# Kernel tuning notes

Hardware: AMD Instinct MI355X
Metric: run time of the kernel (lower is better)

Reference implementation:

```python
import jax, jax.numpy as jnp
import numpy as np

D, H, W, VP = 10, 400, 352, 35  # grid depth/height/width, points per voxel
C1_IN, C1_H = 7, 16   # VFE-1: Linear 7->16, concat -> 32
C2_IN, C2_H = 32, 64  # VFE-2: Linear 32->64, concat -> 128
BN_EPS = 1e-5


def setup_inputs() -> dict:
    key = jax.random.key(0)
    ks = jax.random.split(key, 12)
    K = 15000
    feature = jax.random.normal(ks[0], (K, VP, C1_IN), jnp.float32)
    keep = (jax.random.uniform(ks[1], (K, VP, 1)) < 0.8).astype(jnp.float32)
    feature = feature * keep
    bs = 1
    coordinate = jnp.concatenate([
        jax.random.randint(ks[2], (K, 1), 0, bs),
        jax.random.randint(ks[3], (K, 1), 0, D),
        jax.random.randint(ks[4], (K, 1), 0, H),
        jax.random.randint(ks[5], (K, 1), 0, W),
    ], axis=1).astype(jnp.int32)
    w1 = jax.random.normal(ks[6], (C1_IN, C1_H), jnp.float32) * 0.3
    b1 = jnp.zeros((C1_H,), jnp.float32)
    g1 = jnp.ones((C1_H,), jnp.float32)
    be1 = jnp.zeros((C1_H,), jnp.float32)
    w2 = jax.random.normal(ks[7], (C2_IN, C2_H), jnp.float32) * 0.15
    b2 = jnp.zeros((C2_H,), jnp.float32)
    g2 = jnp.ones((C2_H,), jnp.float32)
    be2 = jnp.zeros((C2_H,), jnp.float32)
    return dict(feature=feature, coordinate=coordinate, bs=bs,
                w1=w1, b1=b1, g1=g1, be1=be1,
                w2=w2, b2=b2, g2=g2, be2=be2)


def _vfe(x, mask, Wm, b, gamma, beta):
    # Linear + ReLU, then BatchNorm1d (training-mode batch stats over (K, VP))
    pw = jax.nn.relu(jnp.einsum('kpi,ih->kph', x, Wm) + b)
    mean = jnp.mean(pw, axis=(0, 1))
    var = jnp.var(pw, axis=(0, 1))  # biased variance, as BN uses for normalization
    pw = (pw - mean) * jax.lax.rsqrt(var + BN_EPS) * gamma + beta
    agg = jnp.max(pw, axis=1, keepdims=True)            # [K,1,Ch] per-voxel max
    concat = jnp.concatenate([pw, jnp.broadcast_to(agg, pw.shape)], axis=-1)
    return concat * mask                                  # mask broadcasts [K,VP,1]


def reference(feature, coordinate, bs, w1, b1, g1, be1, w2, b2, g2, be2):
    # mask: point is valid if max over its 7 features != 0
    mask = (jnp.max(feature, axis=2, keepdims=True) != 0).astype(feature.dtype)
    x = _vfe(feature, mask, w1, b1, g1, be1)   # [K,VP,32]
    x = _vfe(x, mask, w2, b2, g2, be2)         # [K,VP,128]
    voxelwise = jnp.max(x, axis=1)             # [K,128]
    c = coordinate
    out = jnp.zeros((bs, D, H, W, 2 * C2_H), feature.dtype)
    # sparse -> dense sums duplicate coordinates, matching torch.sparse to_dense
    out = out.at[c[:, 0], c[:, 1], c[:, 2], c[:, 3]].add(voxelwise)
    return out
```

## Files before the change

kernel.cpp:

```cpp
#include <hip/hip_runtime.h>
#include <math.h>

#define VPTS 35
#define CIN1 7
#define CH1  16
#define CH2  64
#define DD   10
#define HHH  400
#define WWW  352
#define BN_EPS 1e-5f
#define NSTRIPE 8


__global__ void __launch_bounds__(256) k_stats1(
    const float* __restrict__ feat,
    const float* __restrict__ w1, const float* __restrict__ b1,
    float* __restrict__ red1p, int KP) {
  float w[CIN1][CH1], bb[CH1];
#pragma unroll
  for (int i = 0; i < CIN1; ++i)
#pragma unroll
    for (int c = 0; c < CH1; ++c) w[i][c] = w1[i * CH1 + c];
#pragma unroll
  for (int c = 0; c < CH1; ++c) bb[c] = b1[c];
  float s[CH1], q[CH1];
#pragma unroll
  for (int c = 0; c < CH1; ++c) { s[c] = 0.f; q[c] = 0.f; }
  int tid = blockIdx.x * blockDim.x + threadIdx.x;
  int stride = gridDim.x * blockDim.x;
  for (int idx = tid; idx < KP; idx += stride) {
    float x[CIN1];
#pragma unroll
    for (int i = 0; i < CIN1; ++i) x[i] = feat[(size_t)idx * CIN1 + i];
#pragma unroll
    for (int c = 0; c < CH1; ++c) {
      float a = bb[c];
#pragma unroll
      for (int i = 0; i < CIN1; ++i) a = fmaf(x[i], w[i][c], a);
      a = fmaxf(a, 0.f);
      s[c] += a;
      q[c] = fmaf(a, a, q[c]);
    }
  }
  __shared__ float ssum[2 * CH1];
  if (threadIdx.x < 2 * CH1) ssum[threadIdx.x] = 0.f;
  __syncthreads();
#pragma unroll
  for (int c = 0; c < CH1; ++c) {
    float a = s[c], b = q[c];
    for (int o = 32; o > 0; o >>= 1) {
      a += __shfl_down(a, o);
      b += __shfl_down(b, o);
    }
    if ((threadIdx.x & 63) == 0) {
      atomicAdd(&ssum[c], a);
      atomicAdd(&ssum[CH1 + c], b);
    }
  }
  __syncthreads();
  if (threadIdx.x < 2 * CH1)
    atomicAdd(&red1p[(blockIdx.x & (NSTRIPE - 1)) * 2 * CH1 + threadIdx.x],
              ssum[threadIdx.x]);
}

__global__ void __launch_bounds__(256) k_heavy(
    const float* __restrict__ feat,
    const float* __restrict__ w1, const float* __restrict__ b1,
    const float* __restrict__ g1, const float* __restrict__ be1,
    const float* __restrict__ red1p,
    const float* __restrict__ w2, const float* __restrict__ b2,
    const float* __restrict__ g2,
    float* __restrict__ red2p,
    float* __restrict__ E1buf, float* __restrict__ E2buf,
    float* __restrict__ FLbuf, int K, float invN) {
  __shared__ __align__(16) float fs_s[4][248];
  __shared__ __align__(16) float pw1_s[4][560];
  __shared__ __align__(16) float agg1_s[4][16];
  __shared__ float ss[2 * CH2];
  int t = threadIdx.x, lane = t & 63, w = t >> 6;
  float* fs   = fs_s[w];
  float* pw1  = pw1_s[w];
  float* agg1 = agg1_s[w];

  int c1 = lane & 15;
  float r1s = 0.f, r1q = 0.f;
#pragma unroll
  for (int sIdx = 0; sIdx < NSTRIPE; ++sIdx) {
    r1s += red1p[sIdx * 2 * CH1 + c1];
    r1q += red1p[sIdx * 2 * CH1 + CH1 + c1];
  }
  float mean1 = r1s * invN;
  float var1  = r1q * invN - mean1 * mean1;
  float sc1   = g1[c1] * rsqrtf(var1 + BN_EPS);
  float sh1   = be1[c1] - mean1 * sc1;
  float b1c   = b1[c1];
  float w1r[CIN1];
#pragma unroll
  for (int j = 0; j < CIN1; ++j) w1r[j] = w1[j * CH1 + c1];
  float wcol[32];
#pragma unroll
  for (int i = 0; i < 32; ++i) wcol[i] = w2[i * CH2 + lane];
  float b2c = b2[lane];
  float sgn = (g2[lane] >= 0.f) ? 1.f : -1.f;

  float lsum = 0.f, lsq = 0.f;
  int waveg = blockIdx.x * 4 + w;
  int nwave = gridDim.x * 4;
  for (int k = waveg; k < K; k += nwave) {
    for (int i = lane; i < VPTS * CIN1; i += 64)
      fs[i] = feat[(size_t)k * (VPTS * CIN1) + i];
    bool vbit = false;
    if (lane < VPTS) {
      float m = fs[lane * CIN1];
#pragma unroll
      for (int j = 1; j < CIN1; ++j) m = fmaxf(m, fs[lane * CIN1 + j]);
      vbit = (m != 0.f);
    }
    unsigned long long mbits = __ballot(vbit);
#pragma unroll
    for (int j = 0; j < 9; ++j) {
      int idx = lane + 64 * j;
      if (idx < VPTS * CH1) {
        int p = idx >> 4;
        float a = b1c;
#pragma unroll
        for (int jj = 0; jj < CIN1; ++jj) a = fmaf(fs[p * CIN1 + jj], w1r[jj], a);
        a = fmaxf(a, 0.f);
        pw1[idx] = fmaf(a, sc1, sh1);
      }
    }
    {
      int g = lane >> 4;
      float am = -INFINITY;
      for (int p = g; p < VPTS; p += 4) am = fmaxf(am, pw1[p * CH1 + c1]);
      am = fmaxf(am, __shfl_xor(am, 16));
      am = fmaxf(am, __shfl_xor(am, 32));
      if (lane < CH1) agg1[lane] = am;
    }
    float aggdot = 0.f;
    {
      const float4* a4 = (const float4*)agg1;
#pragma unroll
      for (int i = 0; i < 4; ++i) {
        float4 v = a4[i];
        aggdot = fmaf(v.x, wcol[16 + 4 * i + 0], aggdot);
        aggdot = fmaf(v.y, wcol[16 + 4 * i + 1], aggdot);
        aggdot = fmaf(v.z, wcol[16 + 4 * i + 2], aggdot);
        aggdot = fmaf(v.w, wcol[16 + 4 * i + 3], aggdot);
      }
    }
    float E1w = -INFINITY, E2w = -INFINITY;
    const float4* p4 = (const float4*)pw1;
    for (int p = 0; p < VPTS; ++p) {
      float4 v0 = p4[p * 4 + 0], v1 = p4[p * 4 + 1];
      float4 v2 = p4[p * 4 + 2], v3 = p4[p * 4 + 3];
      float low = 0.f;
      low = fmaf(v0.x, wcol[0], low);  low = fmaf(v0.y, wcol[1], low);
      low = fmaf(v0.z, wcol[2], low);  low = fmaf(v0.w, wcol[3], low);
      low = fmaf(v1.x, wcol[4], low);  low = fmaf(v1.y, wcol[5], low);
      low = fmaf(v1.z, wcol[6], low);  low = fmaf(v1.w, wcol[7], low);
      low = fmaf(v2.x, wcol[8], low);  low = fmaf(v2.y, wcol[9], low);
      low = fmaf(v2.z, wcol[10], low); low = fmaf(v2.w, wcol[11], low);
      low = fmaf(v3.x, wcol[12], low); low = fmaf(v3.y, wcol[13], low);
      low = fmaf(v3.z, wcol[14], low); low = fmaf(v3.w, wcol[15], low);
      bool valid = (mbits >> p) & 1ull;
      float m = valid ? 1.f : 0.f;
      float pw2 = fmaxf(fmaf(m, low + aggdot, b2c), 0.f);
      lsum += pw2;
      lsq = fmaf(pw2, pw2, lsq);
      float sp = sgn * pw2;
      E2w = fmaxf(E2w, sp);
      if (valid) E1w = fmaxf(E1w, sp);
    }
    E1buf[(size_t)k * 64 + lane] = E1w;
    E2buf[(size_t)k * 64 + lane] = E2w;
    if (lane == 0) FLbuf[k] = (float)__popcll(mbits);
  }
  if (t < 2 * CH2) ss[t] = 0.f;
  __syncthreads();
  atomicAdd(&ss[lane], lsum);
  atomicAdd(&ss[CH2 + lane], lsq);
  __syncthreads();
  if (t < 2 * CH2)
    atomicAdd(&red2p[(blockIdx.x & (NSTRIPE - 1)) * 2 * CH2 + t], ss[t]);
}

__global__ void __launch_bounds__(256) k_scatter(
    const float* __restrict__ E1buf, const float* __restrict__ E2buf,
    const float* __restrict__ FLbuf, const float* __restrict__ red2p,
    const float* __restrict__ g2, const float* __restrict__ be2,
    const int* __restrict__ coord, float* __restrict__ out, int K,
    float invN) {
  __shared__ float scsh2_s[2 * CH2];
  int t = threadIdx.x;
  if (t < CH2) {
    float rs = 0.f, rq = 0.f;
#pragma unroll
    for (int sIdx = 0; sIdx < NSTRIPE; ++sIdx) {
      rs += red2p[sIdx * 2 * CH2 + t];
      rq += red2p[sIdx * 2 * CH2 + CH2 + t];
    }
    float mean = rs * invN;
    float var = rq * invN - mean * mean;
    float inv = rsqrtf(var + BN_EPS);
    float sc = g2[t] * inv;
    scsh2_s[t] = sc;
    scsh2_s[CH2 + t] = be2[t] - mean * sc;
  }
  __syncthreads();
  int k = blockIdx.x * 2 + (t >> 7);
  if (k >= K) return;
  int tl = t & 127;
  int c = tl & 63;
  float nv = FLbuf[k];
  bool anyV = nv > 0.f;
  bool anyI = nv < (float)VPTS;
  float sc = scsh2_s[c], sh = scsh2_s[CH2 + c];
  float cand = -INFINITY;
  if (anyV) {
    float E = (tl < 64) ? E1buf[(size_t)k * 64 + c] : E2buf[(size_t)k * 64 + c];
    cand = fmaf(fabsf(sc), E, sh);
  }
  if (anyI) cand = fmaxf(cand, 0.f);
  int4 cc = *reinterpret_cast<const int4*>(coord + (size_t)k * 4);
  long vox = ((long)(cc.x * DD + cc.y) * HHH + cc.z) * WWW + cc.w;
  atomicAdd(&out[vox * (2 * CH2) + tl], cand);
}

__global__ void k_finalize(const float* __restrict__ red,
                           const float* __restrict__ g,
                           const float* __restrict__ be,
                           float* __restrict__ scsh, int CH, float invN) {
  int c = threadIdx.x;
  if (c < CH) {
    float mean = red[c] * invN;
    float var = red[CH + c] * invN - mean * mean;
    float inv = rsqrtf(var + BN_EPS);
    float sc = g[c] * inv;
    scsh[c] = sc;
    scsh[CH + c] = be[c] - mean * sc;
  }
}

__global__ void __launch_bounds__(256) k_stats1_fb(
    const float* __restrict__ feat,
    const float* __restrict__ w1, const float* __restrict__ b1,
    float* __restrict__ red1, int KP) {
  float w[CIN1][CH1], bb[CH1];
#pragma unroll
  for (int i = 0; i < CIN1; ++i)
#pragma unroll
    for (int c = 0; c < CH1; ++c) w[i][c] = w1[i * CH1 + c];
#pragma unroll
  for (int c = 0; c < CH1; ++c) bb[c] = b1[c];
  float s[CH1], q[CH1];
#pragma unroll
  for (int c = 0; c < CH1; ++c) { s[c] = 0.f; q[c] = 0.f; }
  int tid = blockIdx.x * blockDim.x + threadIdx.x;
  int stride = gridDim.x * blockDim.x;
  for (int idx = tid; idx < KP; idx += stride) {
    float x[CIN1];
#pragma unroll
    for (int i = 0; i < CIN1; ++i) x[i] = feat[(size_t)idx * CIN1 + i];
#pragma unroll
    for (int c = 0; c < CH1; ++c) {
      float a = bb[c];
#pragma unroll
      for (int i = 0; i < CIN1; ++i) a = fmaf(x[i], w[i][c], a);
      a = fmaxf(a, 0.f);
      s[c] += a;
      q[c] = fmaf(a, a, q[c]);
    }
  }
  __shared__ float ssum[2 * CH1];
  if (threadIdx.x < 2 * CH1) ssum[threadIdx.x] = 0.f;
  __syncthreads();
#pragma unroll
  for (int c = 0; c < CH1; ++c) {
    float a = s[c], b = q[c];
    for (int o = 32; o > 0; o >>= 1) {
      a += __shfl_down(a, o);
      b += __shfl_down(b, o);
    }
    if ((threadIdx.x & 63) == 0) {
      atomicAdd(&ssum[c], a);
      atomicAdd(&ssum[CH1 + c], b);
    }
  }
  __syncthreads();
  if (threadIdx.x < 2 * CH1) atomicAdd(&red1[threadIdx.x], ssum[threadIdx.x]);
}

__device__ __forceinline__ void compute_x2_old(
    const float* __restrict__ feat, int k, int t,
    const float* __restrict__ w1, const float* __restrict__ b1,
    const float* __restrict__ scsh1,
    float* fs, float* mask_s, float* pw1_s, float* agg1_s, float* x2_s) {
  if (t < VPTS * CIN1) fs[t] = feat[(size_t)k * (VPTS * CIN1) + t];
  __syncthreads();
  if (t < VPTS) {
    float m = fs[t * CIN1];
#pragma unroll
    for (int i = 1; i < CIN1; ++i) m = fmaxf(m, fs[t * CIN1 + i]);
    mask_s[t] = (m != 0.f) ? 1.f : 0.f;
  }
  for (int i = t; i < VPTS * CH1; i += 256) {
    int p = i >> 4, c = i & 15;
    float acc = b1[c];
#pragma unroll
    for (int j = 0; j < CIN1; ++j) acc = fmaf(fs[p * CIN1 + j], w1[j * CH1 + c], acc);
    acc = fmaxf(acc, 0.f);
    pw1_s[i] = fmaf(acc, scsh1[c], scsh1[CH1 + c]);
  }
  __syncthreads();
  if (t < CH1) {
    float m = pw1_s[t];
    for (int p = 1; p < VPTS; ++p) m = fmaxf(m, pw1_s[p * CH1 + t]);
    agg1_s[t] = m;
  }
  __syncthreads();
  for (int i = t; i < VPTS * 32; i += 256) {
    int p = i >> 5, c = i & 31;
    x2_s[i] = (c < CH1 ? pw1_s[p * CH1 + c] : agg1_s[c - CH1]) * mask_s[p];
  }
  __syncthreads();
}

__global__ void __launch_bounds__(256) k_stats2_old(
    const float* __restrict__ feat,
    const float* __restrict__ w1, const float* __restrict__ b1,
    const float* __restrict__ scsh1,
    const float* __restrict__ w2, const float* __restrict__ b2,
    float* __restrict__ red2, int K) {
  __shared__ float fs[VPTS * CIN1], mask_s[VPTS], pw1_s[VPTS * CH1], agg1_s[CH1];
  __shared__ __align__(16) float x2_s[VPTS * 32];
  __shared__ __align__(16) float w2_s[32 * CH2];
  __shared__ float ss[2 * CH2];
  int t = threadIdx.x;
  for (int i = t; i < 32 * CH2; i += 256) w2_s[i] = w2[i];
  if (t < 2 * CH2) ss[t] = 0.f;
  __syncthreads();
  int c = t & 63;
  float wcol[32];
#pragma unroll
  for (int i = 0; i < 32; ++i) wcol[i] = w2_s[i * CH2 + c];
  float bb = b2[c];
  float lsum = 0.f, lsq = 0.f;
  for (int k = blockIdx.x; k < K; k += gridDim.x) {
    compute_x2_old(feat, k, t, w1, b1, scsh1, fs, mask_s, pw1_s, agg1_s, x2_s);
    for (int p = t >> 6; p < VPTS; p += 4) {
      const float4* xv = (const float4*)(x2_s + p * 32);
      float a = bb;
#pragma unroll
      for (int i = 0; i < 8; ++i) {
        float4 v = xv[i];
        a = fmaf(v.x, wcol[4 * i + 0], a);
        a = fmaf(v.y, wcol[4 * i + 1], a);
        a = fmaf(v.z, wcol[4 * i + 2], a);
        a = fmaf(v.w, wcol[4 * i + 3], a);
      }
      a = fmaxf(a, 0.f);
      lsum += a;
      lsq = fmaf(a, a, lsq);
    }
  }
  atomicAdd(&ss[c], lsum);
  atomicAdd(&ss[CH2 + c], lsq);
  __syncthreads();
  if (t < 2 * CH2) atomicAdd(&red2[t], ss[t]);
}

__global__ void __launch_bounds__(256) k_final_old(
    const float* __restrict__ feat,
    const float* __restrict__ w1, const float* __restrict__ b1,
    const float* __restrict__ scsh1,
    const float* __restrict__ w2, const float* __restrict__ b2,
    const float* __restrict__ scsh2,
    const int* __restrict__ coord,
    float* __restrict__ out, int K) {
  __shared__ float fs[VPTS * CIN1], mask_s[VPTS], pw1_s[VPTS * CH1], agg1_s[CH1];
  __shared__ __align__(16) float x2_s[VPTS * 32];
  __shared__ __align__(16) float w2_s[32 * CH2];
  __shared__ float pw2_s[VPTS * CH2];
  __shared__ float agg2_s[CH2];
  int t = threadIdx.x;
  for (int i = t; i < 32 * CH2; i += 256) w2_s[i] = w2[i];
  __syncthreads();
  int c = t & 63;
  float wcol[32];
#pragma unroll
  for (int i = 0; i < 32; ++i) wcol[i] = w2_s[i * CH2 + c];
  float bb = b2[c];
  float sc = scsh2[c], sh = scsh2[CH2 + c];
  for (int k = blockIdx.x; k < K; k += gridDim.x) {
    compute_x2_old(feat, k, t, w1, b1, scsh1, fs, mask_s, pw1_s, agg1_s, x2_s);
    for (int p = t >> 6; p < VPTS; p += 4) {
      const float4* xv = (const float4*)(x2_s + p * 32);
      float a = bb;
#pragma unroll
      for (int i = 0; i < 8; ++i) {
        float4 v = xv[i];
        a = fmaf(v.x, wcol[4 * i + 0], a);
        a = fmaf(v.y, wcol[4 * i + 1], a);
        a = fmaf(v.z, wcol[4 * i + 2], a);
        a = fmaf(v.w, wcol[4 * i + 3], a);
      }
      a = fmaxf(a, 0.f);
      pw2_s[p * CH2 + c] = fmaf(a, sc, sh);
    }
    __syncthreads();
    if (t < CH2) {
      float m = pw2_s[t];
      for (int p = 1; p < VPTS; ++p) m = fmaxf(m, pw2_s[p * CH2 + t]);
      agg2_s[t] = m;
    }
    __syncthreads();
    if (t < 2 * CH2) {
      float vm = -INFINITY;
      if (t < CH2) {
        for (int p = 0; p < VPTS; ++p) vm = fmaxf(vm, pw2_s[p * CH2 + t] * mask_s[p]);
      } else {
        float a = agg2_s[t - CH2];
        for (int p = 0; p < VPTS; ++p) vm = fmaxf(vm, a * mask_s[p]);
      }
      int4 cc = *reinterpret_cast<const int4*>(coord + (size_t)k * 4);
      long vox = ((long)(cc.x * DD + cc.y) * HHH + cc.z) * WWW + cc.w;
      atomicAdd(&out[vox * (2 * CH2) + t], vm);
    }
  }
}

extern "C" void kernel_launch(void* const* d_in, const int* in_sizes, int n_in,
                              void* d_out, int out_size, void* d_ws, size_t ws_size,
                              hipStream_t stream) {
  const float* feat = (const float*)d_in[0];
  const int* coord  = (const int*)d_in[1];
  const float* w1  = (const float*)d_in[3];
  const float* b1  = (const float*)d_in[4];
  const float* g1  = (const float*)d_in[5];
  const float* be1 = (const float*)d_in[6];
  const float* w2  = (const float*)d_in[7];
  const float* b2  = (const float*)d_in[8];
  const float* g2  = (const float*)d_in[9];
  const float* be2 = (const float*)d_in[10];
  float* out = (float*)d_out;
  float* ws = (float*)d_ws;

  int K = in_sizes[0] / (VPTS * CIN1);
  int KP = K * VPTS;
  float invN = 1.f / (float)KP;

  float* red1p = ws;
  float* red2p = ws + 256;
  float* fb    = ws + 1280;
  float* E1buf = ws + 2048;
  float* E2buf = E1buf + (size_t)64 * K;
  float* FLbuf = E2buf + (size_t)64 * K;

  size_t need_bytes = (2048 + (size_t)K * 129) * sizeof(float);

  hipMemsetAsync(out, 0, (size_t)out_size * sizeof(float), stream);
  hipMemsetAsync(ws, 0, 1600 * sizeof(float), stream);

  if (ws_size >= need_bytes) {
    k_stats1<<<512, 256, 0, stream>>>(feat, w1, b1, red1p, KP);
    k_heavy<<<2048, 256, 0, stream>>>(feat, w1, b1, g1, be1, red1p,
                                      w2, b2, g2, red2p, E1buf, E2buf, FLbuf,
                                      K, invN);
    k_scatter<<<(K + 1) / 2, 256, 0, stream>>>(E1buf, E2buf, FLbuf, red2p,
                                               g2, be2, coord, out, K, invN);
  } else {
    float* red1  = fb;
    float* scsh1 = fb + 32;
    float* red2  = fb + 64;
    float* scsh2 = fb + 192;
    k_stats1_fb<<<512, 256, 0, stream>>>(feat, w1, b1, red1, KP);
    k_finalize<<<1, 64, 0, stream>>>(red1, g1, be1, scsh1, CH1, invN);
    k_stats2_old<<<1024, 256, 0, stream>>>(feat, w1, b1, scsh1, w2, b2, red2, K);
    k_finalize<<<1, 64, 0, stream>>>(red2, g2, be2, scsh2, CH2, invN);
    k_final_old<<<2048, 256, 0, stream>>>(feat, w1, b1, scsh1, w2, b2, scsh2,
                                          coord, out, K);
  }
}
```

Before: 187.1 us.

## Fold output zeroing and stat resets into stats kernel, drop atomics

The first-layer stats kernel now runs on only 64 blocks, and each block writes its partial sums to its own slot instead of using striped atomics. k_heavy reduces the 64 per-block slots itself. The remaining blocks of the same launch zero the first 20% of the dense output with float4 stores, and block 0 clears the second-layer reduction buffer. A memset then clears the rest of the output, which removes the separate workspace memset and aims to overlap output zeroing with the stats pass. The risks are fewer blocks doing the stats work and an arbitrary 20% split ratio.

Measured after the change: 197.5 us. 1.06x slower.

```diff
diff --git a/kernel.cpp b/kernel.cpp
--- a/kernel.cpp
+++ b/kernel.cpp
@@ -10,12 +10,25 @@
 #define WWW  352
 #define BN_EPS 1e-5f
 #define NSTRIPE 8
-
-
-__global__ void __launch_bounds__(256) k_stats1(
+#define SB 64
+
+
+__global__ void __launch_bounds__(256) k_A(
     const float* __restrict__ feat,
     const float* __restrict__ w1, const float* __restrict__ b1,
-    float* __restrict__ red1p, int KP) {
+    float* __restrict__ red1w, float* __restrict__ red2p,
+    float4* __restrict__ out4, long zA, int KP) {
+  int t = threadIdx.x;
+  if (blockIdx.x >= SB) {
+    float4 z = make_float4(0.f, 0.f, 0.f, 0.f);
+    long fidx = (long)(blockIdx.x - SB);
+    long stride = (long)(gridDim.x - SB) * 256;
+    for (long zi = fidx * 256 + t; zi < zA; zi += stride) out4[zi] = z;
+    return;
+  }
+  if (blockIdx.x == 0) {
+    for (int i = t; i < NSTRIPE * 2 * CH2; i += 256) red2p[i] = 0.f;
+  }
   float w[CIN1][CH1], bb[CH1];
 #pragma unroll
   for (int i = 0; i < CIN1; ++i)
@@ -26,8 +39,8 @@
   float s[CH1], q[CH1];
 #pragma unroll
   for (int c = 0; c < CH1; ++c) { s[c] = 0.f; q[c] = 0.f; }
-  int tid = blockIdx.x * blockDim.x + threadIdx.x;
-  int stride = gridDim.x * blockDim.x;
+  int tid = blockIdx.x * 256 + t;
+  int stride = SB * 256;
   for (int idx = tid; idx < KP; idx += stride) {
     float x[CIN1];
 #pragma unroll
@@ -43,7 +56,7 @@
     }
   }
   __shared__ float ssum[2 * CH1];
-  if (threadIdx.x < 2 * CH1) ssum[threadIdx.x] = 0.f;
+  if (t < 2 * CH1) ssum[t] = 0.f;
   __syncthreads();
 #pragma unroll
   for (int c = 0; c < CH1; ++c) {
@@ -52,22 +65,20 @@
       a += __shfl_down(a, o);
       b += __shfl_down(b, o);
     }
-    if ((threadIdx.x & 63) == 0) {
+    if ((t & 63) == 0) {
       atomicAdd(&ssum[c], a);
       atomicAdd(&ssum[CH1 + c], b);
     }
   }
   __syncthreads();
-  if (threadIdx.x < 2 * CH1)
-    atomicAdd(&red1p[(blockIdx.x & (NSTRIPE - 1)) * 2 * CH1 + threadIdx.x],
-              ssum[threadIdx.x]);
+  if (t < 2 * CH1) red1w[blockIdx.x * 32 + t] = ssum[t];
 }
 
 __global__ void __launch_bounds__(256) k_heavy(
     const float* __restrict__ feat,
     const float* __restrict__ w1, const float* __restrict__ b1,
     const float* __restrict__ g1, const float* __restrict__ be1,
-    const float* __restrict__ red1p,
+    const float* __restrict__ red1w,
     const float* __restrict__ w2, const float* __restrict__ b2,
     const float* __restrict__ g2,
     float* __restrict__ red2p,
@@ -84,10 +95,10 @@
 
   int c1 = lane & 15;
   float r1s = 0.f, r1q = 0.f;
-#pragma unroll
-  for (int sIdx = 0; sIdx < NSTRIPE; ++sIdx) {
-    r1s += red1p[sIdx * 2 * CH1 + c1];
-    r1q += red1p[sIdx * 2 * CH1 + CH1 + c1];
+#pragma unroll 8
+  for (int sIdx = 0; sIdx < SB; ++sIdx) {
+    r1s += red1w[sIdx * 32 + c1];
+    r1q += red1w[sIdx * 32 + CH1 + c1];
   }
   float mean1 = r1s * invN;
   float var1  = r1q * invN - mean1 * mean1;
@@ -450,21 +461,24 @@
   int KP = K * VPTS;
   float invN = 1.f / (float)KP;
 
-  float* red1p = ws;
-  float* red2p = ws + 256;
-  float* fb    = ws + 1280;
-  float* E1buf = ws + 2048;
+  float* red1w = ws;
+  float* red2p = ws + 2048;
+  float* fb    = ws + 3072;
+  float* E1buf = ws + 4096;
   float* E2buf = E1buf + (size_t)64 * K;
   float* FLbuf = E2buf + (size_t)64 * K;
 
-  size_t need_bytes = (2048 + (size_t)K * 129) * sizeof(float);
-
-  hipMemsetAsync(out, 0, (size_t)out_size * sizeof(float), stream);
-  hipMemsetAsync(ws, 0, 1600 * sizeof(float), stream);
+  size_t need_bytes = (4096 + (size_t)K * 129) * sizeof(float);
+
+  long n4 = (long)out_size / 4;
+  long zA = (n4 * 20) / 100;
 
   if (ws_size >= need_bytes) {
-    k_stats1<<<512, 256, 0, stream>>>(feat, w1, b1, red1p, KP);
-    k_heavy<<<2048, 256, 0, stream>>>(feat, w1, b1, g1, be1, red1p,
+    k_A<<<2048, 256, 0, stream>>>(feat, w1, b1, red1w, red2p,
+                                  (float4*)out, zA, KP);
+    hipMemsetAsync((char*)out + (size_t)zA * 16, 0,
+                   (size_t)out_size * sizeof(float) - (size_t)zA * 16, stream);
+    k_heavy<<<2048, 256, 0, stream>>>(feat, w1, b1, g1, be1, red1w,
                                       w2, b2, g2, red2p, E1buf, E2buf, FLbuf,
                                       K, invN);
     k_scatter<<<(K + 1) / 2, 256, 0, stream>>>(E1buf, E2buf, FLbuf, red2p,
@@ -474,6 +488,8 @@
     float* scsh1 = fb + 32;
     float* red2  = fb + 64;
     float* scsh2 = fb + 192;
+    hipMemsetAsync(out, 0, (size_t)out_size * sizeof(float), stream);
+    hipMemsetAsync(fb, 0, 320 * sizeof(float), stream);
     k_stats1_fb<<<512, 256, 0, stream>>>(feat, w1, b1, red1, KP);
     k_finalize<<<1, 64, 0, stream>>>(red1, g1, be1, scsh1, CH1, invN);
     k_stats2_old<<<1024, 256, 0, stream>>>(feat, w1, b1, scsh1, w2, b2, red2, K);
```
